# Optimization experiments

Hardware: AMD Instinct MI355X
Metric: run time of the kernel (lower is better)

The kernel has to match this reference:

```python
import jax, jax.numpy as jnp
import numpy as np

ALPHA = 0.2  # LeakyReLU negative slope
NEG_INF = -1e9


def setup_inputs() -> dict:
    key = jax.random.key(0)
    k1, k2, k3, k4 = jax.random.split(key, 4)
    B, N, Fin, Fout = 8, 2048, 128, 64
    h = jax.random.normal(k1, (B, N, Fin), dtype=jnp.float32)
    adj_mask = jax.random.randint(k2, (B, N, N), 0, 2).astype(jnp.int32)
    # xavier_uniform-style scales
    W = jax.random.uniform(k3, (Fout, Fin), dtype=jnp.float32,
                           minval=-1.0, maxval=1.0) * np.sqrt(6.0 / (Fin + Fout))
    a = jax.random.uniform(k4, (2 * Fout,), dtype=jnp.float32,
                           minval=-1.0, maxval=1.0) * np.sqrt(6.0 / (2 * Fout + 1))
    return {"h": h, "adj_mask": adj_mask, "W": W, "a": a}


def reference(h, adj_mask, W, a):
    # Wh: [B, N, Fout]
    Wh = jnp.einsum("bnf,of->bno", h, W)
    Fout = Wh.shape[-1]
    a1, a2 = a[:Fout], a[Fout:]
    # additive decomposition of a([Wh_i || Wh_j]): e_ij = leakyrelu(s1_i + s2_j)
    s1 = Wh @ a1  # [B, N]
    s2 = Wh @ a2  # [B, N]
    e = jax.nn.leaky_relu(s1[:, :, None] + s2[:, None, :], negative_slope=ALPHA)  # [B,N,N]
    e = jnp.where(adj_mask == 0, NEG_INF, e)
    attention = jax.nn.softmax(e, axis=-1)
    # dropout is identity in eval mode / p effectively 0 for the reference
    h_prime = jnp.einsum("bij,bjo->bio", attention, Wh)
    return h_prime
```

## Files before the change

kernel.cpp:

```cpp
#include <hip/hip_runtime.h>
#include <hip/hip_fp16.h>
#include <math.h>

#define LRELU_ALPHA 0.2f
#define NEG_INF -1000000000.0f

constexpr int B_ = 8, N_ = 2048, FIN = 128, FOUT = 64;

typedef _Float16 __attribute__((ext_vector_type(8))) f16x8;
typedef float __attribute__((ext_vector_type(4))) f32x4;

__device__ __forceinline__ void gload16(const void* g, void* l) {
  __builtin_amdgcn_global_load_lds(
      (const __attribute__((address_space(1))) void*)g,
      (__attribute__((address_space(3))) void*)l, 16, 0, 0);
}

__global__ __launch_bounds__(256) void k_wh(
    const float* __restrict__ h, const float* __restrict__ W,
    const float* __restrict__ a, unsigned short* __restrict__ WhT,
    float* __restrict__ s1, float* __restrict__ s2) {
  __shared__ float Wt[128][65];
  __shared__ float hs[16][128];

  const int t = threadIdx.x;
  const int row0 = blockIdx.x * 16;

  for (int e = t; e < 64 * 128; e += 256) {
    int o = e >> 7, f = e & 127;
    Wt[f][o] = W[e];
  }
  {
    const float4* hg = (const float4*)(h + (size_t)row0 * FIN);
    for (int i4 = t; i4 < 16 * 32; i4 += 256) {
      int r = i4 >> 5, f4 = i4 & 31;
      *(float4*)&hs[r][f4 * 4] = hg[i4];
    }
  }
  __syncthreads();

  const int wave = t >> 6, lane = t & 63;
  float acc[4] = {0.f, 0.f, 0.f, 0.f};
#pragma unroll 4
  for (int f4 = 0; f4 < 32; ++f4) {
    float w0 = Wt[4 * f4 + 0][lane], w1 = Wt[4 * f4 + 1][lane];
    float w2 = Wt[4 * f4 + 2][lane], w3 = Wt[4 * f4 + 3][lane];
#pragma unroll
    for (int r = 0; r < 4; ++r) {
      float4 hv = *(const float4*)&hs[wave * 4 + r][f4 * 4];
      acc[r] += hv.x * w0 + hv.y * w1 + hv.z * w2 + hv.w * w3;
    }
  }

  const float a1v = a[lane], a2v = a[64 + lane];
  const int b = row0 / N_;
#pragma unroll
  for (int r = 0; r < 4; ++r) {
    const int row = row0 + wave * 4 + r;
    const int n = row - b * N_;
    const float v = acc[r];
    WhT[((size_t)b * 64 + lane) * N_ + n] = __half_as_ushort(__float2half(v));
    float p1 = v * a1v, p2 = v * a2v;
#pragma unroll
    for (int d = 32; d; d >>= 1) {
      p1 += __shfl_xor(p1, d, 64);
      p2 += __shfl_xor(p2, d, 64);
    }
    if (lane == 0) { s1[row] = p1; s2[row] = p2; }
  }
}

__global__ __launch_bounds__(256, 2) void k_attn(
    const unsigned short* __restrict__ WhT,
    const float* __restrict__ s1g, const float* __restrict__ s2g,
    const int* __restrict__ adj, float* __restrict__ out) {
  __shared__ __align__(16) unsigned char sA[16 * 1024];
  __shared__ __align__(16) unsigned char sB[16 * 1024];
  __shared__ float s2s[N_];
  __shared__ float lsum_lds[32];

  const int t = threadIdx.x;
  const int wave = t >> 6, lane = t & 63;
  const int m = lane & 15, q = lane >> 4;
  const int b = blockIdx.y;
  const int i0 = blockIdx.x * 32;
  const int rg = wave & 1;
  const int p0 = (wave >> 1) * 2;

  const int* adjB = adj + (size_t)b * N_ * N_;
  const unsigned short* whB = WhT + (size_t)b * 64 * N_;
  const float* s2R = s2g + b * N_;

  for (int i = t; i < N_ / 4; i += 256)
    ((float4*)s2s)[i] = ((const float4*)s2R)[i];

  const float s1r = s1g[b * N_ + i0 + rg * 16 + m];

  const unsigned char* gp[4];
  int gstr;
  if (wave < 2) {
    const size_t r = (size_t)(i0 + wave * 16 + m);
#pragma unroll
    for (int ii = 0; ii < 4; ++ii) {
      int ks = ii >> 1, hh = ii & 1;
      gp[ii] = (const unsigned char*)(adjB + r * N_ + ks * 32 + q * 8 + hh * 4);
    }
    gstr = 64 * 4;
  } else {
#pragma unroll
    for (int ii = 0; ii < 4; ++ii) {
      int g = (wave - 2) * 2 + (ii >> 1), ks = ii & 1;
      gp[ii] = (const unsigned char*)(whB + (size_t)(g * 16 + m) * N_ +
                                      ks * 32 + q * 8);
    }
    gstr = 64 * 2;
  }

#define STAGE(S, c)                                                       \
  {                                                                       \
    _Pragma("unroll") for (int ii = 0; ii < 4; ++ii)                      \
        gload16(gp[ii] + (size_t)(c) * gstr, (S) + (wave * 4 + ii) * 1024); \
  }

  f32x4 acc0 = {0.f, 0.f, 0.f, 0.f}, acc1 = acc0;
  float lsum = 0.f;

  auto consume = [&](const unsigned char* base, int c) {
#pragma unroll
    for (int ks = 0; ks < 2; ++ks) {
      int4 A0 = *(const int4*)(base + (rg * 4 + ks * 2 + 0) * 1024 + lane * 16);
      int4 A1 = *(const int4*)(base + (rg * 4 + ks * 2 + 1) * 1024 + lane * 16);
      const float* sp = &s2s[c * 64 + ks * 32 + q * 8];
      float4 sv0 = *(const float4*)sp;
      float4 sv1 = *(const float4*)(sp + 4);
      float xs[8] = {sv0.x, sv0.y, sv0.z, sv0.w, sv1.x, sv1.y, sv1.z, sv1.w};
      int avs[8] = {A0.x, A0.y, A0.z, A0.w, A1.x, A1.y, A1.z, A1.w};
      f16x8 af;
#pragma unroll
      for (int j = 0; j < 8; ++j) {
        float x = s1r + xs[j];
        float e = fmaxf(x, LRELU_ALPHA * x);
        e = avs[j] ? (e - 2.0f) : NEG_INF;
        float p = __expf(e);
        lsum += p;
        af[j] = (_Float16)p;
      }
      f16x8 b0 = *(const f16x8*)(base + (8 + (p0 + 0) * 2 + ks) * 1024 + lane * 16);
      f16x8 b1 = *(const f16x8*)(base + (8 + (p0 + 1) * 2 + ks) * 1024 + lane * 16);
      acc0 = __builtin_amdgcn_mfma_f32_16x16x32_f16(af, b0, acc0, 0, 0, 0);
      acc1 = __builtin_amdgcn_mfma_f32_16x16x32_f16(af, b1, acc1, 0, 0, 0);
    }
  };

  STAGE(sA, 0);
  __syncthreads();

  for (int cc = 0; cc < 16; ++cc) {
    const int c0 = 2 * cc, c1 = 2 * cc + 1;
    STAGE(sB, c1);
    consume(sA, c0);
    __syncthreads();
    if (c1 + 1 < 32) STAGE(sA, c1 + 1);
    consume(sB, c1);
    __syncthreads();
  }

  lsum += __shfl_xor(lsum, 16, 64);
  lsum += __shfl_xor(lsum, 32, 64);
  if (wave < 2 && lane < 16) lsum_lds[wave * 16 + lane] = lsum;
  __syncthreads();

#pragma unroll
  for (int r = 0; r < 4; ++r) {
    const int ri = q * 4 + r;
    float l = lsum_lds[rg * 16 + ri];
    float inv = (l == 0.f) ? 1.f : 1.f / l;
    const size_t row = (size_t)b * N_ + i0 + rg * 16 + ri;
    out[row * FOUT + (p0 + 0) * 16 + m] = acc0[r] * inv;
    out[row * FOUT + (p0 + 1) * 16 + m] = acc1[r] * inv;
  }
#undef STAGE
}

extern "C" void kernel_launch(void* const* d_in, const int* in_sizes, int n_in,
                              void* d_out, int out_size, void* d_ws, size_t ws_size,
                              hipStream_t stream) {
  const float* h   = (const float*)d_in[0];
  const int*   adj = (const int*)d_in[1];
  const float* W   = (const float*)d_in[2];
  const float* a   = (const float*)d_in[3];
  float* out = (float*)d_out;

  unsigned short* WhT = (unsigned short*)d_ws;
  float* s1 = (float*)(WhT + (size_t)B_ * 64 * N_);
  float* s2 = s1 + (size_t)B_ * N_;

  k_wh<<<dim3(B_ * N_ / 16), 256, 0, stream>>>(h, W, a, WhT, s1, s2);
  k_attn<<<dim3(N_ / 32, B_), 256, 0, stream>>>(WhT, s1, s2, adj, out);
}
```

Baseline: 226.5 us.

## Replace LDS staging with register-prefetched direct global loads in attention kernel

The attention kernel no longer stages adjacency and WhT tiles through double-buffered LDS with global_load_lds and block barriers. Each wave now loads its own adjacency rows and WhT columns straight into registers, using a 4-slot software prefetch ring. The row-sum is computed with an extra MFMA against a ones vector, which removes the shuffle/LDS reduction, and the leaky-relu arithmetic is folded into two precomputed constants. In exchange, the two waves sharing a row group now both load the same adjacency data, so adjacency global traffic doubles (served by cache at best). Register pressure also rises considerably, and the row sum is now taken from fp16-rounded probabilities.

```diff
diff --git a/kernel.cpp b/kernel.cpp
--- a/kernel.cpp
+++ b/kernel.cpp
@@ -9,12 +9,6 @@
 
 typedef _Float16 __attribute__((ext_vector_type(8))) f16x8;
 typedef float __attribute__((ext_vector_type(4))) f32x4;
-
-__device__ __forceinline__ void gload16(const void* g, void* l) {
-  __builtin_amdgcn_global_load_lds(
-      (const __attribute__((address_space(1))) void*)g,
-      (__attribute__((address_space(3))) void*)l, 16, 0, 0);
-}
 
 __global__ __launch_bounds__(256) void k_wh(
     const float* __restrict__ h, const float* __restrict__ W,
@@ -74,10 +68,7 @@
     const unsigned short* __restrict__ WhT,
     const float* __restrict__ s1g, const float* __restrict__ s2g,
     const int* __restrict__ adj, float* __restrict__ out) {
-  __shared__ __align__(16) unsigned char sA[16 * 1024];
-  __shared__ __align__(16) unsigned char sB[16 * 1024];
   __shared__ float s2s[N_];
-  __shared__ float lsum_lds[32];
 
   const int t = threadIdx.x;
   const int wave = t >> 6, lane = t & 63;
@@ -87,99 +78,93 @@
   const int rg = wave & 1;
   const int p0 = (wave >> 1) * 2;
 
-  const int* adjB = adj + (size_t)b * N_ * N_;
-  const unsigned short* whB = WhT + (size_t)b * 64 * N_;
-  const float* s2R = s2g + b * N_;
-
-  for (int i = t; i < N_ / 4; i += 256)
-    ((float4*)s2s)[i] = ((const float4*)s2R)[i];
-
-  const float s1r = s1g[b * N_ + i0 + rg * 16 + m];
-
-  const unsigned char* gp[4];
-  int gstr;
-  if (wave < 2) {
-    const size_t r = (size_t)(i0 + wave * 16 + m);
-#pragma unroll
-    for (int ii = 0; ii < 4; ++ii) {
-      int ks = ii >> 1, hh = ii & 1;
-      gp[ii] = (const unsigned char*)(adjB + r * N_ + ks * 32 + q * 8 + hh * 4);
-    }
-    gstr = 64 * 4;
-  } else {
-#pragma unroll
-    for (int ii = 0; ii < 4; ++ii) {
-      int g = (wave - 2) * 2 + (ii >> 1), ks = ii & 1;
-      gp[ii] = (const unsigned char*)(whB + (size_t)(g * 16 + m) * N_ +
-                                      ks * 32 + q * 8);
-    }
-    gstr = 64 * 2;
+  {
+    const float4* s2R = (const float4*)(s2g + (size_t)b * N_);
+    for (int i = t; i < N_ / 4; i += 256) ((float4*)s2s)[i] = s2R[i];
   }
 
-#define STAGE(S, c)                                                       \
-  {                                                                       \
-    _Pragma("unroll") for (int ii = 0; ii < 4; ++ii)                      \
-        gload16(gp[ii] + (size_t)(c) * gstr, (S) + (wave * 4 + ii) * 1024); \
+  const int row_i = i0 + rg * 16 + m;
+  const int* adjR = adj + (size_t)b * N_ * N_ + (size_t)row_i * N_;
+  const unsigned short* whB = WhT + (size_t)b * 64 * N_;
+  const unsigned short* bp0 = whB + (size_t)((p0 + 0) * 16 + m) * N_ + q * 8;
+  const unsigned short* bp1 = whB + (size_t)((p0 + 1) * 16 + m) * N_ + q * 8;
+
+  const float s1r = s1g[b * N_ + row_i];
+  const float c1 = s1r - 2.0f;
+  const float c2 = LRELU_ALPHA * s1r - 2.0f;
+
+  f16x8 ones;
+#pragma unroll
+  for (int j = 0; j < 8; ++j) ones[j] = (_Float16)1.0f;
+
+  __syncthreads();
+
+  f32x4 acc0 = {0.f, 0.f, 0.f, 0.f}, acc1 = acc0, accS = acc0;
+
+#define DECL_SLOT(P) int4 P##a0, P##a1, P##a2, P##a3; \
+                     f16x8 P##b0, P##b1, P##b2, P##b3;
+#define LOAD(P, c) {                                                     \
+    const int* ap = adjR + (c) * 64 + q * 8;                             \
+    P##a0 = *(const int4*)ap;                                            \
+    P##a1 = *(const int4*)(ap + 4);                                      \
+    P##a2 = *(const int4*)(ap + 32);                                     \
+    P##a3 = *(const int4*)(ap + 36);                                     \
+    P##b0 = *(const f16x8*)(bp0 + (c) * 64);                             \
+    P##b1 = *(const f16x8*)(bp0 + (c) * 64 + 32);                        \
+    P##b2 = *(const f16x8*)(bp1 + (c) * 64);                             \
+    P##b3 = *(const f16x8*)(bp1 + (c) * 64 + 32);                        \
+  }
+#define ELEM8(af, AV0, AV1, SA, SB) {                                    \
+    int av[8] = {AV0.x, AV0.y, AV0.z, AV0.w, AV1.x, AV1.y, AV1.z, AV1.w};\
+    float xs[8] = {SA.x, SA.y, SA.z, SA.w, SB.x, SB.y, SB.z, SB.w};      \
+    _Pragma("unroll") for (int j = 0; j < 8; ++j) {                      \
+      float e = fmaxf(c1 + xs[j], fmaf(LRELU_ALPHA, xs[j], c2));         \
+      e = av[j] ? e : NEG_INF;                                           \
+      af[j] = (_Float16)__expf(e);            \
+    }                                                                    \
+  }
+#define CONSUME(P, c) {                                                  \
+    const float* sp = s2s + (c) * 64 + q * 8;                            \
+    float4 s0a = *(const float4*)sp;                                     \
+    float4 s0b = *(const float4*)(sp + 4);                               \
+    float4 s1a = *(const float4*)(sp + 32);                              \
+    float4 s1b = *(const float4*)(sp + 36);                              \
+    f16x8 af0, af1;                                                      \
+    ELEM8(af0, P##a0, P##a1, s0a, s0b);                                  \
+    ELEM8(af1, P##a2, P##a3, s1a, s1b);                                  \
+    acc0 = __builtin_amdgcn_mfma_f32_16x16x32_f16(af0, P##b0, acc0, 0, 0, 0); \
+    acc1 = __builtin_amdgcn_mfma_f32_16x16x32_f16(af0, P##b2, acc1, 0, 0, 0); \
+    accS = __builtin_amdgcn_mfma_f32_16x16x32_f16(af0, ones, accS, 0, 0, 0);  \
+    acc0 = __builtin_amdgcn_mfma_f32_16x16x32_f16(af1, P##b1, acc0, 0, 0, 0); \
+    acc1 = __builtin_amdgcn_mfma_f32_16x16x32_f16(af1, P##b3, acc1, 0, 0, 0); \
+    accS = __builtin_amdgcn_mfma_f32_16x16x32_f16(af1, ones, accS, 0, 0, 0);  \
   }
 
-  f32x4 acc0 = {0.f, 0.f, 0.f, 0.f}, acc1 = acc0;
-  float lsum = 0.f;
+  DECL_SLOT(u) DECL_SLOT(v) DECL_SLOT(w) DECL_SLOT(x)
+  LOAD(u, 0) LOAD(v, 1) LOAD(w, 2) LOAD(x, 3)
 
-  auto consume = [&](const unsigned char* base, int c) {
-#pragma unroll
-    for (int ks = 0; ks < 2; ++ks) {
-      int4 A0 = *(const int4*)(base + (rg * 4 + ks * 2 + 0) * 1024 + lane * 16);
-      int4 A1 = *(const int4*)(base + (rg * 4 + ks * 2 + 1) * 1024 + lane * 16);
-      const float* sp = &s2s[c * 64 + ks * 32 + q * 8];
-      float4 sv0 = *(const float4*)sp;
-      float4 sv1 = *(const float4*)(sp + 4);
-      float xs[8] = {sv0.x, sv0.y, sv0.z, sv0.w, sv1.x, sv1.y, sv1.z, sv1.w};
-      int avs[8] = {A0.x, A0.y, A0.z, A0.w, A1.x, A1.y, A1.z, A1.w};
-      f16x8 af;
-#pragma unroll
-      for (int j = 0; j < 8; ++j) {
-        float x = s1r + xs[j];
-        float e = fmaxf(x, LRELU_ALPHA * x);
-        e = avs[j] ? (e - 2.0f) : NEG_INF;
-        float p = __expf(e);
-        lsum += p;
-        af[j] = (_Float16)p;
-      }
-      f16x8 b0 = *(const f16x8*)(base + (8 + (p0 + 0) * 2 + ks) * 1024 + lane * 16);
-      f16x8 b1 = *(const f16x8*)(base + (8 + (p0 + 1) * 2 + ks) * 1024 + lane * 16);
-      acc0 = __builtin_amdgcn_mfma_f32_16x16x32_f16(af, b0, acc0, 0, 0, 0);
-      acc1 = __builtin_amdgcn_mfma_f32_16x16x32_f16(af, b1, acc1, 0, 0, 0);
-    }
-  };
-
-  STAGE(sA, 0);
-  __syncthreads();
-
-  for (int cc = 0; cc < 16; ++cc) {
-    const int c0 = 2 * cc, c1 = 2 * cc + 1;
-    STAGE(sB, c1);
-    consume(sA, c0);
-    __syncthreads();
-    if (c1 + 1 < 32) STAGE(sA, c1 + 1);
-    consume(sB, c1);
-    __syncthreads();
+  for (int cc = 0; cc < 8; ++cc) {
+    const int c = 4 * cc;
+    const int cn = (cc < 7) ? c + 4 : c;
+    CONSUME(u, c + 0) LOAD(u, cn + 0)
+    CONSUME(v, c + 1) LOAD(v, cn + 1)
+    CONSUME(w, c + 2) LOAD(w, cn + 2)
+    CONSUME(x, c + 3) LOAD(x, cn + 3)
   }
-
-  lsum += __shfl_xor(lsum, 16, 64);
-  lsum += __shfl_xor(lsum, 32, 64);
-  if (wave < 2 && lane < 16) lsum_lds[wave * 16 + lane] = lsum;
-  __syncthreads();
 
 #pragma unroll
   for (int r = 0; r < 4; ++r) {
     const int ri = q * 4 + r;
-    float l = lsum_lds[rg * 16 + ri];
-    float inv = (l == 0.f) ? 1.f : 1.f / l;
+    const float l = accS[r];
+    const float inv = (l == 0.f) ? 1.f : 1.f / l;
     const size_t row = (size_t)b * N_ + i0 + rg * 16 + ri;
     out[row * FOUT + (p0 + 0) * 16 + m] = acc0[r] * inv;
     out[row * FOUT + (p0 + 1) * 16 + m] = acc1[r] * inv;
   }
-#undef STAGE
+#undef DECL_SLOT
+#undef LOAD
+#undef ELEM8
+#undef CONSUME
 }
 
 extern "C" void kernel_launch(void* const* d_in, const int* in_sizes, int n_in,
```

Measured after the change: 273.2 us. 1.21x slower.

## Quad-buffer attention staging with vmcnt waits, MFMA row sums, exp2 folding

Applied to the files above, without the earlier changes.

Replaces the two-buffer LDS pipeline with four buffers kept three chunks ahead, using explicit s_waitcnt vmcnt and bare barriers in place of __syncthreads. The softmax row sum now comes from an extra MFMA against a ones vector instead of scalar accumulation plus a shuffle/LDS reduction. The exponent is rewritten as exp2 with log2(e) and the -2 shift folded into precomputed constants and the pre-scaled s2. The aim is more memory latency hiding and fewer VALU ops per element. In exchange it raises LDS use, which may reduce occupancy, and the hand-written vmcnt counts must match the issued loads exactly for correctness.

```diff
diff --git a/kernel.cpp b/kernel.cpp
--- a/kernel.cpp
+++ b/kernel.cpp
@@ -4,6 +4,7 @@
 
 #define LRELU_ALPHA 0.2f
 #define NEG_INF -1000000000.0f
+#define L2E 1.44269504088896340736f
 
 constexpr int B_ = 8, N_ = 2048, FIN = 128, FOUT = 64;
 
@@ -74,10 +75,8 @@
     const unsigned short* __restrict__ WhT,
     const float* __restrict__ s1g, const float* __restrict__ s2g,
     const int* __restrict__ adj, float* __restrict__ out) {
-  __shared__ __align__(16) unsigned char sA[16 * 1024];
-  __shared__ __align__(16) unsigned char sB[16 * 1024];
+  __shared__ __align__(16) unsigned char sbuf[4][16 * 1024];
   __shared__ float s2s[N_];
-  __shared__ float lsum_lds[32];
 
   const int t = threadIdx.x;
   const int wave = t >> 6, lane = t & 63;
@@ -89,12 +88,23 @@
 
   const int* adjB = adj + (size_t)b * N_ * N_;
   const unsigned short* whB = WhT + (size_t)b * 64 * N_;
-  const float* s2R = s2g + b * N_;
-
-  for (int i = t; i < N_ / 4; i += 256)
-    ((float4*)s2s)[i] = ((const float4*)s2R)[i];
+
+  {
+    const float4* s2R = (const float4*)(s2g + (size_t)b * N_);
+    for (int i = t; i < N_ / 4; i += 256) {
+      float4 v = s2R[i];
+      v.x *= L2E; v.y *= L2E; v.z *= L2E; v.w *= L2E;
+      ((float4*)s2s)[i] = v;
+    }
+  }
 
   const float s1r = s1g[b * N_ + i0 + rg * 16 + m];
+  const float c1 = (s1r - 2.0f) * L2E;
+  const float c2 = (LRELU_ALPHA * s1r - 2.0f) * L2E;
+
+  f16x8 ones;
+#pragma unroll
+  for (int j = 0; j < 8; ++j) ones[j] = (_Float16)1.0f;
 
   const unsigned char* gp[4];
   int gstr;
@@ -122,8 +132,7 @@
         gload16(gp[ii] + (size_t)(c) * gstr, (S) + (wave * 4 + ii) * 1024); \
   }
 
-  f32x4 acc0 = {0.f, 0.f, 0.f, 0.f}, acc1 = acc0;
-  float lsum = 0.f;
+  f32x4 acc0 = {0.f, 0.f, 0.f, 0.f}, acc1 = acc0, accS = acc0;
 
   auto consume = [&](const unsigned char* base, int c) {
 #pragma unroll
@@ -138,43 +147,48 @@
       f16x8 af;
 #pragma unroll
       for (int j = 0; j < 8; ++j) {
-        float x = s1r + xs[j];
-        float e = fmaxf(x, LRELU_ALPHA * x);
-        e = avs[j] ? (e - 2.0f) : NEG_INF;
-        float p = __expf(e);
-        lsum += p;
-        af[j] = (_Float16)p;
+        float x = xs[j];
+        float e = fmaxf(c1 + x, fmaf(LRELU_ALPHA, x, c2));
+        e = avs[j] ? e : NEG_INF;
+        af[j] = (_Float16)__builtin_amdgcn_exp2f(e);
       }
       f16x8 b0 = *(const f16x8*)(base + (8 + (p0 + 0) * 2 + ks) * 1024 + lane * 16);
       f16x8 b1 = *(const f16x8*)(base + (8 + (p0 + 1) * 2 + ks) * 1024 + lane * 16);
       acc0 = __builtin_amdgcn_mfma_f32_16x16x32_f16(af, b0, acc0, 0, 0, 0);
       acc1 = __builtin_amdgcn_mfma_f32_16x16x32_f16(af, b1, acc1, 0, 0, 0);
+      accS = __builtin_amdgcn_mfma_f32_16x16x32_f16(af, ones, accS, 0, 0, 0);
     }
   };
 
-  STAGE(sA, 0);
+  STAGE(sbuf[0], 0)
+  STAGE(sbuf[1], 1)
+  STAGE(sbuf[2], 2)
   __syncthreads();
 
-  for (int cc = 0; cc < 16; ++cc) {
-    const int c0 = 2 * cc, c1 = 2 * cc + 1;
-    STAGE(sB, c1);
-    consume(sA, c0);
-    __syncthreads();
-    if (c1 + 1 < 32) STAGE(sA, c1 + 1);
-    consume(sB, c1);
-    __syncthreads();
-  }
-
-  lsum += __shfl_xor(lsum, 16, 64);
-  lsum += __shfl_xor(lsum, 32, 64);
-  if (wave < 2 && lane < 16) lsum_lds[wave * 16 + lane] = lsum;
-  __syncthreads();
+  consume(sbuf[0], 0);
+  STAGE(sbuf[3], 3)
+
+  for (int c = 1; c <= 28; ++c) {
+    asm volatile("s_waitcnt vmcnt(8)" ::: "memory");
+    __builtin_amdgcn_s_barrier();
+    consume(sbuf[c & 3], c);
+    STAGE(sbuf[(c + 3) & 3], c + 3)
+  }
+  asm volatile("s_waitcnt vmcnt(8)" ::: "memory");
+  __builtin_amdgcn_s_barrier();
+  consume(sbuf[1], 29);
+  asm volatile("s_waitcnt vmcnt(4)" ::: "memory");
+  __builtin_amdgcn_s_barrier();
+  consume(sbuf[2], 30);
+  asm volatile("s_waitcnt vmcnt(0)" ::: "memory");
+  __builtin_amdgcn_s_barrier();
+  consume(sbuf[3], 31);
 
 #pragma unroll
   for (int r = 0; r < 4; ++r) {
     const int ri = q * 4 + r;
-    float l = lsum_lds[rg * 16 + ri];
-    float inv = (l == 0.f) ? 1.f : 1.f / l;
+    const float l = accS[r];
+    const float inv = (l == 0.f) ? 1.f : 1.f / l;
     const size_t row = (size_t)b * N_ + i0 + rg * 16 + ri;
     out[row * FOUT + (p0 + 0) * 16 + m] = acc0[r] * inv;
     out[row * FOUT + (p0 + 1) * 16 + m] = acc1[r] * inv;
```

After: 222.5 us. No clear change (-1.7%).
